# Kernel optimization log

Hardware: AMD Instinct MI355X
Metric: run time of the kernel (lower is better)

The kernel has to match this reference:

```python
import jax, jax.numpy as jnp
import numpy as np

B, S, H, D = 2, 2048, 8, 64
W = 128  # attention window radius


def setup_inputs() -> dict:
    key = jax.random.key(0)
    kq, kk, kv = jax.random.split(key, 3)
    return {
        "query": jax.random.normal(kq, (B, S, H, D), dtype=jnp.float32),
        "key": jax.random.normal(kk, (B, S, H, D), dtype=jnp.float32),
        "value": jax.random.normal(kv, (B, S, H, D), dtype=jnp.float32),
        "window_size": W,
    }


def reference(query, key, value, window_size):
    # Sliding-window (symmetric, radius=window_size, inclusive) attention.
    # Per-query softmax over keys j with |i - j| <= window_size, scale 1/sqrt(D).
    b, s, h, d = query.shape
    scale = 1.0 / jnp.sqrt(jnp.asarray(d, query.dtype))
    # scores: [B, H, S, S]
    scores = jnp.einsum("bihd,bjhd->bhij", query * scale, key)
    i = jnp.arange(s)[:, None]
    j = jnp.arange(s)[None, :]
    band = jnp.abs(i - j) <= window_size  # [S, S]
    scores = jnp.where(band, scores, -jnp.inf)
    weights = jax.nn.softmax(scores, axis=-1)
    out = jnp.einsum("bhij,bjhd->bihd", weights, value)
    return out
```

## Files before the change

### kernel.cpp

```cpp
#include <hip/hip_runtime.h>
#include <hip/hip_fp16.h>
#include <math.h>

typedef _Float16 half8 __attribute__((ext_vector_type(8)));
typedef _Float16 half4 __attribute__((ext_vector_type(4)));
typedef float f32x4 __attribute__((ext_vector_type(4)));

#define S_LEN 2048
#define NH 8
#define DH 64
#define HD (NH*DH)
#define BQ 64
#define SPAN (BQ + 256)
#define NT 256
#define SPLIT_T 6

__global__ __launch_bounds__(NT, 2)
void swa_mfma(const float* __restrict__ qg, const float* __restrict__ kg,
              const float* __restrict__ vg, const int* __restrict__ wptr,
              float* __restrict__ outg)
{
    __shared__ __align__(16) unsigned short Kl[SPAN * DH];
    __shared__ __align__(16) unsigned short Vt[DH * SPAN];

    int W = *wptr; if (W > 128) W = 128;

    const int t = threadIdx.x;
    int bid = blockIdx.x;
    bid = (bid & 7) * (gridDim.x >> 3) + (bid >> 3);
    const int qt = bid & 31, h = (bid >> 5) & 7, b = bid >> 8;
    const int i0 = qt * BQ, s0 = i0 - W;

    const float* kbh = kg + (size_t)b * S_LEN * HD + h * DH;
    const float* vbh = vg + (size_t)b * S_LEN * HD + h * DH;

    const int wid = t >> 6, lane = t & 63, c = lane & 15, g = lane >> 4;
    const int q = i0 + wid * 16 + c;

    const float* qrow = qg + (size_t)b * S_LEN * HD + h * DH + (size_t)q * HD;
    const f32x4 qf0 = *(const f32x4*)(qrow + g * 8);
    const f32x4 qf1 = *(const f32x4*)(qrow + g * 8 + 4);
    const f32x4 qf2 = *(const f32x4*)(qrow + 32 + g * 8);
    const f32x4 qf3 = *(const f32x4*)(qrow + 32 + g * 8 + 4);

    #pragma unroll
    for (int it = 0; it < 6; ++it) {
        const int task = t + it * NT;
        const int koff = task >> 3, cr = task & 7;
        const int j = s0 + koff;
        f32x4 f0 = {0,0,0,0}, f1 = {0,0,0,0};
        if ((unsigned)j < S_LEN) {
            const float* p = kbh + (size_t)j * HD + cr * 8;
            f0 = *(const f32x4*)p; f1 = *(const f32x4*)(p + 4);
        }
        half8 hv;
        #pragma unroll
        for (int e = 0; e < 4; ++e) { hv[e] = (_Float16)f0[e]; hv[4+e] = (_Float16)f1[e]; }
        *(half8*)(&Kl[koff * 64 + ((cr ^ (koff & 7)) << 3)]) = hv;
    }
    #pragma unroll
    for (int it = 0; it < 3; ++it) {
        const int task = t + it * NT;
        const int kq = task >> 4, dq = task & 15;
        f32x4 r[4];
        #pragma unroll
        for (int jj = 0; jj < 4; ++jj) {
            const int j = s0 + kq * 4 + jj;
            f32x4 f = {0,0,0,0};
            if ((unsigned)j < S_LEN) f = *(const f32x4*)(vbh + (size_t)j * HD + dq * 4);
            r[jj] = f;
        }
        #pragma unroll
        for (int i = 0; i < 4; ++i) {
            const int dim = dq * 4 + i;
            half4 w = { (_Float16)r[0][i], (_Float16)r[1][i],
                        (_Float16)r[2][i], (_Float16)r[3][i] };
            *(half4*)(&Vt[dim * SPAN + (((kq >> 1) ^ (dim & 7)) << 3) + ((kq & 1) << 2)]) = w;
        }
    }

    half8 qa0, qa1;
    {
        const float qs = 0.18033688011112042f;
        #pragma unroll
        for (int e = 0; e < 4; ++e) {
            qa0[e] = (_Float16)(qf0[e] * qs); qa0[4+e] = (_Float16)(qf1[e] * qs);
            qa1[e] = (_Float16)(qf2[e] * qs); qa1[4+e] = (_Float16)(qf3[e] * qs);
        }
    }

    const int c7 = c & 7;
    const int ch0 = (g ^ c7) << 3;
    const int ch1 = ((g + 4) ^ c7) << 3;
    int lo = q - W; if (lo < 0) lo = 0;
    int hi = q + W; if (hi > S_LEN - 1) hi = S_LEN - 1;
    const unsigned rng = (unsigned)(hi - lo);

    int ts = wid >> 1;
    const int ts0 = (s0 < 0) ? ((-s0) >> 5) : 0;
    if (ts0 > ts) ts = ts0;
    const int te_w = (16 * wid + 15 + 2 * W) >> 5;
    const int te_s = (S_LEN - 1 - s0) >> 5;
    const int te = te_w < te_s ? te_w : te_s;

    float m = -1e4f, l = 0.f;
    f32x4 o0 = {0,0,0,0}, o1 = {0,0,0,0}, o2 = {0,0,0,0}, o3 = {0,0,0,0};

    __syncthreads();

    f32x4 kpf[4][2];
    #pragma unroll
    for (int it = 0; it < 4; ++it) {
        const int task = 1536 + t + it * NT;
        const int koff = task >> 3, cr = task & 7;
        const int j = s0 + koff;
        f32x4 f0 = {0,0,0,0}, f1 = {0,0,0,0};
        if ((unsigned)j < S_LEN) {
            const float* p = kbh + (size_t)j * HD + cr * 8;
            f0 = *(const f32x4*)p; f1 = *(const f32x4*)(p + 4);
        }
        kpf[it][0] = f0; kpf[it][1] = f1;
    }
    f32x4 vpf[2][4];
    #pragma unroll
    for (int it = 0; it < 2; ++it) {
        const int task = 768 + t + it * NT;
        const int kq = task >> 4, dq = task & 15;
        #pragma unroll
        for (int jj = 0; jj < 4; ++jj) {
            const int j = s0 + kq * 4 + jj;
            f32x4 f = {0,0,0,0};
            if ((unsigned)j < S_LEN) f = *(const f32x4*)(vbh + (size_t)j * HD + dq * 4);
            vpf[it][jj] = f;
        }
    }

    auto computeTile = [&](int t32) {
        const unsigned short* krow = &Kl[(t32 * 32 + c) * 64];
        half8 k00 = *(const half8*)(krow + ch0);
        half8 k01 = *(const half8*)(krow + ch1);
        half8 k10 = *(const half8*)(krow + 16 * 64 + ch0);
        half8 k11 = *(const half8*)(krow + 16 * 64 + ch1);
        f32x4 st0 = {0,0,0,0}, st1 = {0,0,0,0};
        __builtin_amdgcn_s_setprio(1);
        st0 = __builtin_amdgcn_mfma_f32_16x16x32_f16(k00, qa0, st0, 0, 0, 0);
        st0 = __builtin_amdgcn_mfma_f32_16x16x32_f16(k01, qa1, st0, 0, 0, 0);
        st1 = __builtin_amdgcn_mfma_f32_16x16x32_f16(k10, qa0, st1, 0, 0, 0);
        st1 = __builtin_amdgcn_mfma_f32_16x16x32_f16(k11, qa1, st1, 0, 0, 0);
        __builtin_amdgcn_s_setprio(0);

        const int kb = s0 + t32 * 32 + 4 * g;
        float sv0[4], sv1[4];
        #pragma unroll
        for (int r = 0; r < 4; ++r) {
            sv0[r] = ((unsigned)(kb + r - lo) <= rng)      ? st0[r] : -30000.f;
            sv1[r] = ((unsigned)(kb + 16 + r - lo) <= rng) ? st1[r] : -30000.f;
        }
        float tmax = fmaxf(fmaxf(fmaxf(sv0[0], sv0[1]), fmaxf(sv0[2], sv0[3])),
                           fmaxf(fmaxf(sv1[0], sv1[1]), fmaxf(sv1[2], sv1[3])));
        tmax = fmaxf(tmax, __shfl_xor(tmax, 16));
        tmax = fmaxf(tmax, __shfl_xor(tmax, 32));
        if (__any(tmax > m)) {
            const float newm = fmaxf(m, tmax);
            const float alpha = exp2f(m - newm);
            m = newm;
            l *= alpha;
            o0 *= alpha; o1 *= alpha; o2 *= alpha; o3 *= alpha;
        }
        float p0[4], p1[4], ls = 0.f;
        #pragma unroll
        for (int r = 0; r < 4; ++r) {
            p0[r] = exp2f(sv0[r] - m);
            p1[r] = exp2f(sv1[r] - m);
            ls += p0[r] + p1[r];
        }
        l += ls;
        half8 pb;
        #pragma unroll
        for (int r = 0; r < 4; ++r) { pb[r] = (_Float16)p0[r]; pb[4+r] = (_Float16)p1[r]; }

        const int cb = 4 * t32 + (g >> 1);
        const int off1 = ((cb ^ c7) << 3) + ((g & 1) << 2);
        const int off2 = (((cb + 2) ^ c7) << 3) + ((g & 1) << 2);
        __builtin_amdgcn_s_setprio(1);
#define PV_STEP(DF, OACC) { \
        const unsigned short* vrow = &Vt[(16 * DF + c) * SPAN]; \
        half4 vlo = *(const half4*)(vrow + off1); \
        half4 vhi = *(const half4*)(vrow + off2); \
        half8 vf; \
        vf[0]=vlo[0]; vf[1]=vlo[1]; vf[2]=vlo[2]; vf[3]=vlo[3]; \
        vf[4]=vhi[0]; vf[5]=vhi[1]; vf[6]=vhi[2]; vf[7]=vhi[3]; \
        OACC = __builtin_amdgcn_mfma_f32_16x16x32_f16(vf, pb, OACC, 0, 0, 0); }
        PV_STEP(0, o0)
        PV_STEP(1, o1)
        PV_STEP(2, o2)
        PV_STEP(3, o3)
#undef PV_STEP
        __builtin_amdgcn_s_setprio(0);
    };

    for (int t32 = ts; t32 <= te && t32 < SPLIT_T; ++t32) computeTile(t32);

    #pragma unroll
    for (int it = 0; it < 4; ++it) {
        const int task = 1536 + t + it * NT;
        const int koff = task >> 3, cr = task & 7;
        half8 hv;
        #pragma unroll
        for (int e = 0; e < 4; ++e) { hv[e] = (_Float16)kpf[it][0][e]; hv[4+e] = (_Float16)kpf[it][1][e]; }
        *(half8*)(&Kl[koff * 64 + ((cr ^ (koff & 7)) << 3)]) = hv;
    }
    #pragma unroll
    for (int it = 0; it < 2; ++it) {
        const int task = 768 + t + it * NT;
        const int kq = task >> 4, dq = task & 15;
        #pragma unroll
        for (int i = 0; i < 4; ++i) {
            const int dim = dq * 4 + i;
            half4 w = { (_Float16)vpf[it][0][i], (_Float16)vpf[it][1][i],
                        (_Float16)vpf[it][2][i], (_Float16)vpf[it][3][i] };
            *(half4*)(&Vt[dim * SPAN + (((kq >> 1) ^ (dim & 7)) << 3) + ((kq & 1) << 2)]) = w;
        }
    }
    __syncthreads();

    for (int t32 = (ts > SPLIT_T ? ts : SPLIT_T); t32 <= te; ++t32) computeTile(t32);

    l += __shfl_xor(l, 16);
    l += __shfl_xor(l, 32);
    const float inv = 1.0f / l;
    float* orow = outg + (size_t)b * S_LEN * HD + h * DH + (size_t)q * HD + 4 * g;
    { float4 w; w.x=o0[0]*inv; w.y=o0[1]*inv; w.z=o0[2]*inv; w.w=o0[3]*inv; *(float4*)(orow)      = w; }
    { float4 w; w.x=o1[0]*inv; w.y=o1[1]*inv; w.z=o1[2]*inv; w.w=o1[3]*inv; *(float4*)(orow + 16) = w; }
    { float4 w; w.x=o2[0]*inv; w.y=o2[1]*inv; w.z=o2[2]*inv; w.w=o2[3]*inv; *(float4*)(orow + 32) = w; }
    { float4 w; w.x=o3[0]*inv; w.y=o3[1]*inv; w.z=o3[2]*inv; w.w=o3[3]*inv; *(float4*)(orow + 48) = w; }
}

extern "C" void kernel_launch(void* const* d_in, const int* in_sizes, int n_in,
                              void* d_out, int out_size, void* d_ws, size_t ws_size,
                              hipStream_t stream) {
    const float* q = (const float*)d_in[0];
    const float* k = (const float*)d_in[1];
    const float* v = (const float*)d_in[2];
    const int*   w = (const int*)d_in[3];
    float* out = (float*)d_out;

    const int nblocks = 2 * NH * (S_LEN / BQ);
    swa_mfma<<<dim3(nblocks), dim3(NT), 0, stream>>>(q, k, v, w, out);
}
```

Before: 20.84 us.

## Pre-convert K/V to swizzled fp16 workspace and DMA tiles into LDS

A new prep kernel converts K to fp16 and V to a transposed fp16 layout, both pre-swizzled, and writes them to a workspace. The attention kernel then loads its K and V tiles straight into LDS with global_load_lds instead of converting fp32 data per block. This removes the conversion work that overlapping blocks repeat on the same rows and halves the bytes each block fetches. The two-phase prefetch split is dropped in favour of a single sync and one loop. In exchange it adds a second launch and a full fp32-read plus fp16-write pass over K and V through the workspace.

```diff
diff --git a/kernel.cpp b/kernel.cpp
--- a/kernel.cpp
+++ b/kernel.cpp
@@ -5,6 +5,7 @@
 typedef _Float16 half8 __attribute__((ext_vector_type(8)));
 typedef _Float16 half4 __attribute__((ext_vector_type(4)));
 typedef float f32x4 __attribute__((ext_vector_type(4)));
+typedef unsigned short u16x8 __attribute__((ext_vector_type(8)));
 
 #define S_LEN 2048
 #define NH 8
@@ -13,15 +14,68 @@
 #define BQ 64
 #define SPAN (BQ + 256)
 #define NT 256
-#define SPLIT_T 6
+
+__global__ __launch_bounds__(256)
+void swa_prep(const float* __restrict__ kg, const float* __restrict__ vg,
+              unsigned short* __restrict__ kws, unsigned short* __restrict__ vtws)
+{
+    __shared__ unsigned short Vl[64 * 64];
+
+    const int bid = blockIdx.x;
+    const int sb = bid & 31, h = (bid >> 5) & 7, b = bid >> 8;
+    const int t = threadIdx.x;
+
+    const float* kin = kg + (((size_t)b * S_LEN + sb * 64) * NH + h) * DH;
+    const float* vin = vg + (((size_t)b * S_LEN + sb * 64) * NH + h) * DH;
+    unsigned short* kout = kws + ((size_t)(b * NH + h) * S_LEN + sb * 64) * DH;
+
+    #pragma unroll
+    for (int it = 0; it < 2; ++it) {
+        const int task = t + it * 256;
+        const int row = task >> 3, cr = task & 7;
+        const int s = sb * 64 + row;
+        const f32x4 f0 = *(const f32x4*)(kin + (size_t)row * HD + cr * 8);
+        const f32x4 f1 = *(const f32x4*)(kin + (size_t)row * HD + cr * 8 + 4);
+        half8 hv;
+        #pragma unroll
+        for (int e = 0; e < 4; ++e) { hv[e] = (_Float16)f0[e]; hv[4+e] = (_Float16)f1[e]; }
+        *(half8*)(&kout[(size_t)row * DH + ((cr ^ (s & 7)) << 3)]) = hv;
+    }
+
+    #pragma unroll
+    for (int it = 0; it < 2; ++it) {
+        const int task = t + it * 256;
+        const int row = task >> 3, cr = task & 7;
+        const f32x4 f0 = *(const f32x4*)(vin + (size_t)row * HD + cr * 8);
+        const f32x4 f1 = *(const f32x4*)(vin + (size_t)row * HD + cr * 8 + 4);
+        half8 hv;
+        #pragma unroll
+        for (int e = 0; e < 4; ++e) { hv[e] = (_Float16)f0[e]; hv[4+e] = (_Float16)f1[e]; }
+        *(half8*)(&Vl[row * 64 + cr * 8]) = hv;
+    }
+    __syncthreads();
+
+    unsigned short* vtout = vtws + (size_t)(b * NH + h) * DH * S_LEN;
+    #pragma unroll
+    for (int it = 0; it < 2; ++it) {
+        const int task = t + it * 256;
+        const int d = task & 63, kc = task >> 6;
+        u16x8 w;
+        #pragma unroll
+        for (int r = 0; r < 8; ++r) w[r] = Vl[(kc * 8 + r) * 64 + d];
+        *(u16x8*)(&vtout[(size_t)d * S_LEN + ((sb * 8 + (kc ^ (d & 7))) << 3)]) = w;
+    }
+}
 
 __global__ __launch_bounds__(NT, 2)
-void swa_mfma(const float* __restrict__ qg, const float* __restrict__ kg,
-              const float* __restrict__ vg, const int* __restrict__ wptr,
+void swa_mfma(const float* __restrict__ qg,
+              const unsigned short* __restrict__ kws,
+              const unsigned short* __restrict__ vtws,
+              const int* __restrict__ wptr,
               float* __restrict__ outg)
 {
-    __shared__ __align__(16) unsigned short Kl[SPAN * DH];
-    __shared__ __align__(16) unsigned short Vt[DH * SPAN];
+    __shared__ __align__(1024) unsigned short Kl[SPAN * DH];
+    __shared__ __align__(1024) unsigned short Vt[DH * SPAN];
 
     int W = *wptr; if (W > 128) W = 128;
 
@@ -31,54 +85,37 @@
     const int qt = bid & 31, h = (bid >> 5) & 7, b = bid >> 8;
     const int i0 = qt * BQ, s0 = i0 - W;
 
-    const float* kbh = kg + (size_t)b * S_LEN * HD + h * DH;
-    const float* vbh = vg + (size_t)b * S_LEN * HD + h * DH;
-
     const int wid = t >> 6, lane = t & 63, c = lane & 15, g = lane >> 4;
     const int q = i0 + wid * 16 + c;
+
+    const char* kpan = (const char*)(kws + (size_t)(b * NH + h) * S_LEN * DH);
+    const char* vpan = (const char*)(vtws + (size_t)(b * NH + h) * DH * S_LEN);
+    {
+        #pragma unroll
+        for (int i = 0; i < 10; ++i) {
+            const int off = wid * 10240 + i * 1024 + lane * 16;
+            int srow = s0 + (off >> 7);
+            srow = srow < 0 ? 0 : (srow > S_LEN - 1 ? S_LEN - 1 : srow);
+            const void* src = kpan + (size_t)srow * 128 + (off & 127);
+            __builtin_amdgcn_global_load_lds(src, (char*)Kl + wid * 10240 + i * 1024, 16, 0, 0);
+        }
+        #pragma unroll
+        for (int i = 0; i < 10; ++i) {
+            const int off = wid * 10240 + i * 1024 + lane * 16;
+            const int d = off / 640;
+            const int cbyte = off - d * 640;
+            int rb = s0 * 2 + cbyte;
+            rb = rb < 0 ? 0 : (rb > 4080 ? 4080 : rb);
+            const void* src = vpan + (size_t)d * 4096 + rb;
+            __builtin_amdgcn_global_load_lds(src, (char*)Vt + wid * 10240 + i * 1024, 16, 0, 0);
+        }
+    }
 
     const float* qrow = qg + (size_t)b * S_LEN * HD + h * DH + (size_t)q * HD;
     const f32x4 qf0 = *(const f32x4*)(qrow + g * 8);
     const f32x4 qf1 = *(const f32x4*)(qrow + g * 8 + 4);
     const f32x4 qf2 = *(const f32x4*)(qrow + 32 + g * 8);
     const f32x4 qf3 = *(const f32x4*)(qrow + 32 + g * 8 + 4);
-
-    #pragma unroll
-    for (int it = 0; it < 6; ++it) {
-        const int task = t + it * NT;
-        const int koff = task >> 3, cr = task & 7;
-        const int j = s0 + koff;
-        f32x4 f0 = {0,0,0,0}, f1 = {0,0,0,0};
-        if ((unsigned)j < S_LEN) {
-            const float* p = kbh + (size_t)j * HD + cr * 8;
-            f0 = *(const f32x4*)p; f1 = *(const f32x4*)(p + 4);
-        }
-        half8 hv;
-        #pragma unroll
-        for (int e = 0; e < 4; ++e) { hv[e] = (_Float16)f0[e]; hv[4+e] = (_Float16)f1[e]; }
-        *(half8*)(&Kl[koff * 64 + ((cr ^ (koff & 7)) << 3)]) = hv;
-    }
-    #pragma unroll
-    for (int it = 0; it < 3; ++it) {
-        const int task = t + it * NT;
-        const int kq = task >> 4, dq = task & 15;
-        f32x4 r[4];
-        #pragma unroll
-        for (int jj = 0; jj < 4; ++jj) {
-            const int j = s0 + kq * 4 + jj;
-            f32x4 f = {0,0,0,0};
-            if ((unsigned)j < S_LEN) f = *(const f32x4*)(vbh + (size_t)j * HD + dq * 4);
-            r[jj] = f;
-        }
-        #pragma unroll
-        for (int i = 0; i < 4; ++i) {
-            const int dim = dq * 4 + i;
-            half4 w = { (_Float16)r[0][i], (_Float16)r[1][i],
-                        (_Float16)r[2][i], (_Float16)r[3][i] };
-            *(half4*)(&Vt[dim * SPAN + (((kq >> 1) ^ (dim & 7)) << 3) + ((kq & 1) << 2)]) = w;
-        }
-    }
-
     half8 qa0, qa1;
     {
         const float qs = 0.18033688011112042f;
@@ -108,34 +145,7 @@
 
     __syncthreads();
 
-    f32x4 kpf[4][2];
-    #pragma unroll
-    for (int it = 0; it < 4; ++it) {
-        const int task = 1536 + t + it * NT;
-        const int koff = task >> 3, cr = task & 7;
-        const int j = s0 + koff;
-        f32x4 f0 = {0,0,0,0}, f1 = {0,0,0,0};
-        if ((unsigned)j < S_LEN) {
-            const float* p = kbh + (size_t)j * HD + cr * 8;
-            f0 = *(const f32x4*)p; f1 = *(const f32x4*)(p + 4);
-        }
-        kpf[it][0] = f0; kpf[it][1] = f1;
-    }
-    f32x4 vpf[2][4];
-    #pragma unroll
-    for (int it = 0; it < 2; ++it) {
-        const int task = 768 + t + it * NT;
-        const int kq = task >> 4, dq = task & 15;
-        #pragma unroll
-        for (int jj = 0; jj < 4; ++jj) {
-            const int j = s0 + kq * 4 + jj;
-            f32x4 f = {0,0,0,0};
-            if ((unsigned)j < S_LEN) f = *(const f32x4*)(vbh + (size_t)j * HD + dq * 4);
-            vpf[it][jj] = f;
-        }
-    }
-
-    auto computeTile = [&](int t32) {
+    for (int t32 = ts; t32 <= te; ++t32) {
         const unsigned short* krow = &Kl[(t32 * 32 + c) * 64];
         half8 k00 = *(const half8*)(krow + ch0);
         half8 k01 = *(const half8*)(krow + ch1);
@@ -197,34 +207,7 @@
         PV_STEP(3, o3)
 #undef PV_STEP
         __builtin_amdgcn_s_setprio(0);
-    };
-
-    for (int t32 = ts; t32 <= te && t32 < SPLIT_T; ++t32) computeTile(t32);
-
-    #pragma unroll
-    for (int it = 0; it < 4; ++it) {
-        const int task = 1536 + t + it * NT;
-        const int koff = task >> 3, cr = task & 7;
-        half8 hv;
-        #pragma unroll
-        for (int e = 0; e < 4; ++e) { hv[e] = (_Float16)kpf[it][0][e]; hv[4+e] = (_Float16)kpf[it][1][e]; }
-        *(half8*)(&Kl[koff * 64 + ((cr ^ (koff & 7)) << 3)]) = hv;
-    }
-    #pragma unroll
-    for (int it = 0; it < 2; ++it) {
-        const int task = 768 + t + it * NT;
-        const int kq = task >> 4, dq = task & 15;
-        #pragma unroll
-        for (int i = 0; i < 4; ++i) {
-            const int dim = dq * 4 + i;
-            half4 w = { (_Float16)vpf[it][0][i], (_Float16)vpf[it][1][i],
-                        (_Float16)vpf[it][2][i], (_Float16)vpf[it][3][i] };
-            *(half4*)(&Vt[dim * SPAN + (((kq >> 1) ^ (dim & 7)) << 3) + ((kq & 1) << 2)]) = w;
-        }
-    }
-    __syncthreads();
-
-    for (int t32 = (ts > SPLIT_T ? ts : SPLIT_T); t32 <= te; ++t32) computeTile(t32);
+    }
 
     l += __shfl_xor(l, 16);
     l += __shfl_xor(l, 32);
@@ -245,6 +228,9 @@
     const int*   w = (const int*)d_in[3];
     float* out = (float*)d_out;
 
-    const int nblocks = 2 * NH * (S_LEN / BQ);
-    swa_mfma<<<dim3(nblocks), dim3(NT), 0, stream>>>(q, k, v, w, out);
+    unsigned short* kws  = (unsigned short*)d_ws;
+    unsigned short* vtws = kws + (size_t)2 * NH * S_LEN * DH;
+
+    swa_prep<<<dim3(512), dim3(256), 0, stream>>>(k, v, kws, vtws);
+    swa_mfma<<<dim3(2 * NH * (S_LEN / BQ)), dim3(NT), 0, stream>>>(q, kws, vtws, w, out);
 }
```

New measurement: 24.58 us. 1.18x slower.
